# Kernel optimization log

Hardware: AMD Instinct MI355X
Metric: run time of the kernel (lower is better)

## Reference

```python
import jax, jax.numpy as jnp
import numpy as np

N_WIN = 7
NUM_HEADS = 8
DIM = 256
QK = 256
TOPK = 4
MLP_HID = 4 * DIM
SCALE = QK ** -0.5  # used for both region routing and pixel attention (qk_scale=None)


def _layernorm(x, g, b, eps=1e-6):
    mu = jnp.mean(x, axis=-1, keepdims=True)
    var = jnp.mean(jnp.square(x - mu), axis=-1, keepdims=True)
    return (x - mu) * jax.lax.rsqrt(var + eps) * g + b


def _dwconv(x, w, b):
    # x: NHWC, w: (5,5,1,C) depthwise kernel (torch Conv2d groups=C, padding=2)
    y = jax.lax.conv_general_dilated(
        x, w, window_strides=(1, 1), padding='SAME',
        feature_group_count=x.shape[-1],
        dimension_numbers=('NHWC', 'HWIO', 'NHWC'))
    return y + b


def _bra(x, qkv_w, qkv_b, lepe_w, lepe_b, wo_w, wo_b):
    # BiLevelRoutingAttention, NHWC in/out
    N, H, W, C = x.shape
    j = i = N_WIN
    h, w = H // j, W // i
    p2, w2, m = j * i, h * w, NUM_HEADS
    dq, dv = QK // m, C // m
    # window partition: (N, p2, h, w, C)
    xw = x.reshape(N, j, h, i, w, C).transpose(0, 1, 3, 2, 4, 5).reshape(N, p2, h, w, C)
    qkv = xw @ qkv_w + qkv_b
    q = qkv[..., :QK]            # (N,p2,h,w,QK)
    kv = qkv[..., QK:]           # (N,p2,h,w,QK+C)
    q_pix = q.reshape(N, p2, w2, QK)
    kv_pix = kv.reshape(N, p2, w2, QK + C)
    q_win = jnp.mean(q, axis=(2, 3))                    # (N,p2,QK)
    k_win = jnp.mean(kv[..., :QK], axis=(2, 3))         # (N,p2,QK)
    # LePE: depthwise conv on V in full-image layout
    v_img = kv[..., QK:].reshape(N, j, i, h, w, C).transpose(0, 1, 3, 2, 4, 5).reshape(N, H, W, C)
    lepe = _dwconv(v_img, lepe_w, lepe_b)
    # region-to-region routing, top-k window selection
    logit = jnp.einsum('npc,nqc->npq', q_win * SCALE, k_win)    # (N,p2,p2)
    _, r_idx = jax.lax.top_k(logit, TOPK)                       # (N,p2,TOPK)
    # gather KV of selected windows: (N,p2,TOPK,w2,QK+C)
    kv_sel = kv_pix[jnp.arange(N)[:, None, None], r_idx]
    k_sel = kv_sel[..., :QK].reshape(N, p2, TOPK * w2, m, dq).transpose(0, 1, 3, 2, 4)  # (N,p2,m,kw2,dq)
    v_sel = kv_sel[..., QK:].reshape(N, p2, TOPK * w2, m, dv).transpose(0, 1, 3, 2, 4)  # (N,p2,m,kw2,dv)
    q_h = q_pix.reshape(N, p2, w2, m, dq).transpose(0, 1, 3, 2, 4)                      # (N,p2,m,w2,dq)
    aw = jnp.einsum('npmqd,npmkd->npmqk', q_h * SCALE, k_sel)
    aw = jax.nn.softmax(aw, axis=-1)
    out = jnp.einsum('npmqk,npmkd->npmqd', aw, v_sel)           # (N,p2,m,w2,dv)
    out = out.transpose(0, 1, 3, 2, 4).reshape(N, j, i, h, w, C)
    out = out.transpose(0, 1, 3, 2, 4, 5).reshape(N, H, W, C)
    out = out + lepe
    return out @ wo_w + wo_b


def setup_inputs() -> dict:
    key = jax.random.key(0)
    ks = jax.random.split(key, 8)
    s = 0.02
    return {
        'x': jax.random.normal(ks[0], (8, 56, 56, DIM), dtype=jnp.float32),
        'ln1_g': jnp.ones((DIM,), jnp.float32),
        'ln1_b': jnp.zeros((DIM,), jnp.float32),
        'qkv_w': jax.random.normal(ks[1], (DIM, 2 * QK + DIM), jnp.float32) * s,
        'qkv_b': jnp.zeros((2 * QK + DIM,), jnp.float32),
        'lepe_w': jax.random.normal(ks[2], (5, 5, 1, DIM), jnp.float32) * s,
        'lepe_b': jnp.zeros((DIM,), jnp.float32),
        'wo_w': jax.random.normal(ks[3], (DIM, DIM), jnp.float32) * s,
        'wo_b': jnp.zeros((DIM,), jnp.float32),
        'ln2_g': jnp.ones((DIM,), jnp.float32),
        'ln2_b': jnp.zeros((DIM,), jnp.float32),
        'mlp_w1': jax.random.normal(ks[4], (DIM, MLP_HID), jnp.float32) * s,
        'mlp_b1': jnp.zeros((MLP_HID,), jnp.float32),
        'mlp_w2': jax.random.normal(ks[5], (MLP_HID, DIM), jnp.float32) * s,
        'mlp_b2': jnp.zeros((DIM,), jnp.float32),
    }


def reference(x, ln1_g, ln1_b, qkv_w, qkv_b, lepe_w, lepe_b, wo_w, wo_b,
              ln2_g, ln2_b, mlp_w1, mlp_b1, mlp_w2, mlp_b2):
    x = x + _bra(_layernorm(x, ln1_g, ln1_b), qkv_w, qkv_b, lepe_w, lepe_b, wo_w, wo_b)
    h = _layernorm(x, ln2_g, ln2_b)
    h = jax.nn.gelu(h @ mlp_w1 + mlp_b1, approximate=False) @ mlp_w2 + mlp_b2
    return x + h
```

## Files before the change

kernel.cpp:

```cpp
#include <hip/hip_runtime.h>
#include <hip/hip_bf16.h>

#define NIMG 8
#define HW 56
#define CDIM 256
#define TOK (NIMG*HW*HW)
#define NWIN 49
#define NPW (NIMG*NWIN)
#define ATT_SCALE 0.0625f

typedef __attribute__((ext_vector_type(8))) short short8;
typedef __attribute__((ext_vector_type(4))) short short4v;
typedef __attribute__((ext_vector_type(4))) float f32x4;

static const size_t OFF_WQKV  = 0;
static const size_t OFF_WWO   = 393216;
static const size_t OFF_W1    = 524288;
static const size_t OFF_W2    = 1048576;
static const size_t OFF_XLN   = 1572864;
static const size_t OFF_QKV   = 14417920;
static const size_t OFF_QKWIN = 52953088;
static const size_t OFF_RIDX  = 53755904;
static const size_t OFF_ATTN  = 53762176;

__device__ __forceinline__ float gelu_exact(float v) {
    return 0.5f * v * (1.f + erff(v * 0.70710678118654752f));
}
__device__ __forceinline__ short f2bs(float x) {
    __hip_bfloat16 h = __float2bfloat16(x);
    return *(short*)&h;
}
__device__ __forceinline__ float bs2f(short s) {
    return __uint_as_float(((unsigned)(unsigned short)s) << 16);
}
__device__ __forceinline__ void gld16(const short* g, short* l) {
    __builtin_amdgcn_global_load_lds(
        (const __attribute__((address_space(1))) void*)g,
        (__attribute__((address_space(3))) void*)l, 16, 0, 0);
}

__global__ __launch_bounds__(256) void transpose_cast4_k(const float* __restrict__ s0,
                                                         const float* __restrict__ s1,
                                                         const float* __restrict__ s2,
                                                         const float* __restrict__ s3,
                                                         __hip_bfloat16* __restrict__ d0,
                                                         __hip_bfloat16* __restrict__ d1,
                                                         __hip_bfloat16* __restrict__ d2,
                                                         __hip_bfloat16* __restrict__ d3) {
    int b = blockIdx.x;
    const float* src; __hip_bfloat16* dst; int K, N, l;
    if (b < 192)      { src = s0; dst = d0; K = 256;  N = 768;  l = b; }
    else if (b < 256) { src = s1; dst = d1; K = 256;  N = 256;  l = b - 192; }
    else if (b < 512) { src = s2; dst = d2; K = 256;  N = 1024; l = b - 256; }
    else              { src = s3; dst = d3; K = 1024; N = 256;  l = b - 512; }
    int nx = N / 32;
    int n0 = (l % nx) * 32, k0 = (l / nx) * 32;
    __shared__ float t[32][33];
    int tx = threadIdx.x & 31, ty = threadIdx.x >> 5;
    #pragma unroll
    for (int i = 0; i < 32; i += 8)
        t[ty + i][tx] = src[(size_t)(k0 + ty + i) * N + n0 + tx];
    __syncthreads();
    #pragma unroll
    for (int i = 0; i < 32; i += 8)
        dst[(size_t)(n0 + ty + i) * K + k0 + tx] = __float2bfloat16(t[tx][ty + i]);
}

__global__ __launch_bounds__(256) void ln_bf_k(const float* __restrict__ in,
                                               const float* __restrict__ g,
                                               const float* __restrict__ b,
                                               short* __restrict__ out, int remap) {
    int t = blockIdx.x * 4 + (threadIdx.x >> 6);
    int lane = threadIdx.x & 63;
    float4 v = *(const float4*)(in + (size_t)t * 256 + lane * 4);
    float s = v.x + v.y + v.z + v.w;
    float s2 = v.x * v.x + v.y * v.y + v.z * v.z + v.w * v.w;
    #pragma unroll
    for (int o = 32; o > 0; o >>= 1) {
        s  += __shfl_xor(s, o);
        s2 += __shfl_xor(s2, o);
    }
    float mu = s * (1.f / 256.f);
    float rstd = rsqrtf(s2 * (1.f / 256.f) - mu * mu + 1e-6f);
    float4 gv = *(const float4*)(g + lane * 4);
    float4 bv = *(const float4*)(b + lane * 4);
    short4v o;
    o[0] = f2bs((v.x - mu) * rstd * gv.x + bv.x);
    o[1] = f2bs((v.y - mu) * rstd * gv.y + bv.y);
    o[2] = f2bs((v.z - mu) * rstd * gv.z + bv.z);
    o[3] = f2bs((v.w - mu) * rstd * gv.w + bv.w);
    size_t tb;
    if (remap) {
        int n = t / 3136, rem = t % 3136, y = rem / 56, x = rem % 56;
        int p = (y >> 3) * 7 + (x >> 3);
        int si = (y & 7) * 8 + (x & 7);
        tb = (size_t)(n * 49 + p) * 64 + si;
    } else {
        tb = (size_t)t;
    }
    *(short4v*)(out + tb * 256 + lane * 4) = o;
}

__device__ __forceinline__ void mfma_step(const short* As, const short* Bs,
                                          int wm, int wn, int l15, int swr,
                                          f32x4 acc[2][4]) {
    short8 af[2], bfr[4];
    #pragma unroll
    for (int i = 0; i < 2; ++i)
        af[i] = *(const short8*)&As[(wm + i * 16 + l15) * 32 + swr];
    #pragma unroll
    for (int j = 0; j < 4; ++j)
        bfr[j] = *(const short8*)&Bs[(wn + j * 16 + l15) * 32 + swr];
    #pragma unroll
    for (int i = 0; i < 2; ++i)
        #pragma unroll
        for (int j = 0; j < 4; ++j)
            acc[i][j] = __builtin_amdgcn_mfma_f32_16x16x32_bf16(af[i], bfr[j], acc[i][j], 0, 0, 0);
}

template<int MODE>
__global__ __launch_bounds__(256) void gemm64(const short* __restrict__ A,
                                              const short* __restrict__ Bt,
                                              const float* __restrict__ bias,
                                              const float* __restrict__ res,
                                              void* Cv, float* __restrict__ winptr,
                                              int M, int N, int K) {
    const int bn = blockIdx.x * 128;
    const int bm = blockIdx.y * 64;
    const int tid = threadIdx.x;
    const int wave = tid >> 6, lane = tid & 63;
    const int l15 = lane & 15, quad = lane >> 4;
    const int wm = (wave & 1) * 32, wn = (wave >> 1) * 64;

    __shared__ __align__(16) short smem[18432];

    f32x4 acc[2][4];
    #pragma unroll
    for (int i = 0; i < 2; ++i)
        #pragma unroll
        for (int j = 0; j < 4; ++j) acc[i][j] = (f32x4){0.f, 0.f, 0.f, 0.f};

    const int srow = lane >> 2;
    const int scg  = ((lane & 3) ^ ((lane >> 3) & 3)) * 8;
    const short* ga  = A  + (size_t)(bm + wave * 16 + srow) * K + scg;
    const short* gb0 = Bt + (size_t)(bn + wave * 16 + srow) * K + scg;
    const short* gb1 = gb0 + (size_t)64 * K;
    const int swr = (quad ^ ((l15 >> 1) & 3)) * 8;

    const int nt = K >> 5;

    {
        short* b0 = smem;
        gld16(ga,       b0 + wave * 512);
        gld16(gb0,      b0 + 2048 + wave * 512);
        gld16(gb1,      b0 + 4096 + wave * 512);
        short* b1 = smem + 6144;
        gld16(ga  + 32, b1 + wave * 512);
        gld16(gb0 + 32, b1 + 2048 + wave * 512);
        gld16(gb1 + 32, b1 + 4096 + wave * 512);
    }

    for (int t = 0; t < nt; ++t) {
        if (t == nt - 1) asm volatile("s_waitcnt vmcnt(0)" ::: "memory");
        else             asm volatile("s_waitcnt vmcnt(3)" ::: "memory");
        __builtin_amdgcn_s_barrier();
        asm volatile("" ::: "memory");
        if (t + 2 < nt) {
            short* b = smem + ((t + 2) % 3) * 6144;
            int kk = (t + 2) * 32;
            gld16(ga  + kk, b + wave * 512);
            gld16(gb0 + kk, b + 2048 + wave * 512);
            gld16(gb1 + kk, b + 4096 + wave * 512);
        }
        const short* As = smem + (t % 3) * 6144;
        mfma_step(As, As + 2048, wm, wn, l15, swr, acc);
    }

    if (MODE == 0) {
        if (bn < 512) {
            float* wmean = (float*)&smem[12288];
            #pragma unroll
            for (int j = 0; j < 4; ++j) {
                float s = 0.f;
                #pragma unroll
                for (int i = 0; i < 2; ++i)
                    #pragma unroll
                    for (int r = 0; r < 4; ++r) s += acc[i][j][r];
                s += __shfl_xor(s, 16);
                s += __shfl_xor(s, 32);
                if (quad == 0) wmean[wave * 64 + j * 16 + l15] = s;
            }
            __syncthreads();
            if (tid < 128) {
                int c = tid;
                float s = (c < 64) ? (wmean[c] + wmean[64 + c])
                                   : (wmean[64 + c] + wmean[128 + c]);
                int col = bn + c;
                if (col < 512)
                    winptr[(size_t)blockIdx.y * 512 + col] = s * (1.f / 64.f) + bias[col];
            }
        }
    }

    if (MODE == 1) {
        #pragma unroll
        for (int i = 0; i < 2; ++i) {
            int row = bm + wm + i * 16 + quad * 4;
            #pragma unroll
            for (int j = 0; j < 4; ++j) {
                int col = bn + wn + j * 16 + l15;
                float bia = bias[col];
                #pragma unroll
                for (int r = 0; r < 4; ++r) {
                    size_t idx = (size_t)(row + r) * N + col;
                    ((float*)Cv)[idx] = acc[i][j][r] + bia + res[idx];
                }
            }
        }
    } else {
        asm volatile("s_waitcnt lgkmcnt(0)" ::: "memory");
        __builtin_amdgcn_s_barrier();
        asm volatile("" ::: "memory");
        float biasv[4];
        #pragma unroll
        for (int j = 0; j < 4; ++j) biasv[j] = bias[bn + wn + j * 16 + l15];
        short* ep = &smem[wave * 1280];
        short* outp = (short*)Cv;
        #pragma unroll
        for (int p = 0; p < 2; ++p) {
            #pragma unroll
            for (int i = 0; i < 2; ++i)
                #pragma unroll
                for (int jj = 0; jj < 2; ++jj) {
                    int j = p * 2 + jj;
                    #pragma unroll
                    for (int r = 0; r < 4; ++r) {
                        float v = acc[i][j][r] + biasv[j];
                        if (MODE == 2) v = gelu_exact(v);
                        ep[(i * 16 + quad * 4 + r) * 40 + jj * 16 + l15] = f2bs(v);
                    }
                }
            __builtin_amdgcn_s_waitcnt(0);
            int c = lane & 3;
            #pragma unroll
            for (int rr = 0; rr < 2; ++rr) {
                int row = rr * 16 + (lane >> 2);
                short8 v = *(const short8*)&ep[row * 40 + c * 8];
                *(short8*)&outp[(size_t)(bm + wm + row) * N + bn + wn + p * 32 + c * 8] = v;
            }
            __builtin_amdgcn_s_waitcnt(0);
        }
    }
}

__global__ __launch_bounds__(256) void gemm_woln_k(const short* __restrict__ A,
                                                   const short* __restrict__ Bt,
                                                   const float* __restrict__ bias,
                                                   const float* __restrict__ res,
                                                   const float* __restrict__ g2,
                                                   const float* __restrict__ b2,
                                                   float* __restrict__ out,
                                                   short* __restrict__ h2) {
    const int K = 256;
    const int bm = blockIdx.x * 64;
    const int tid = threadIdx.x;
    const int wave = tid >> 6, lane = tid & 63;
    const int l15 = lane & 15, quad = lane >> 4;
    const int wn = wave * 64;

    __shared__ __align__(16) short smem[30720];

    f32x4 acc[4][4];
    #pragma unroll
    for (int i = 0; i < 4; ++i)
        #pragma unroll
        for (int j = 0; j < 4; ++j) acc[i][j] = (f32x4){0.f, 0.f, 0.f, 0.f};

    const int srow = lane >> 2;
    const int scg  = ((lane & 3) ^ ((lane >> 3) & 3)) * 8;
    const short* ga  = A  + (size_t)(bm + wave * 16 + srow) * K + scg;
    const short* gb  = Bt + (size_t)(wn + srow) * K + scg;
    const int swr = (quad ^ ((l15 >> 1) & 3)) * 8;

    const int nt = 8;

    #define WOLN_STAGE(T) do {                                              \
        short* _b = smem + ((T) % 3) * 10240;                               \
        int _kk = (T) * 32;                                                 \
        gld16(ga + _kk, _b + wave * 512);                                   \
        _Pragma("unroll")                                                   \
        for (int X = 0; X < 4; ++X)                                         \
            gld16(gb + (size_t)X * 16 * K + _kk,                            \
                  _b + 2048 + (wave * 4 + X) * 512);                        \
    } while (0)

    WOLN_STAGE(0);
    WOLN_STAGE(1);

    for (int t = 0; t < nt; ++t) {
        if (t == nt - 1) asm volatile("s_waitcnt vmcnt(0)" ::: "memory");
        else             asm volatile("s_waitcnt vmcnt(5)" ::: "memory");
        __builtin_amdgcn_s_barrier();
        asm volatile("" ::: "memory");
        if (t + 2 < nt) WOLN_STAGE(t + 2);
        const short* As = smem + (t % 3) * 10240;
        const short* Bs = As + 2048;
        short8 af[4], bfr[4];
        #pragma unroll
        for (int i = 0; i < 4; ++i)
            af[i] = *(const short8*)&As[(i * 16 + l15) * 32 + swr];
        #pragma unroll
        for (int j = 0; j < 4; ++j)
            bfr[j] = *(const short8*)&Bs[(wn + j * 16 + l15) * 32 + swr];
        #pragma unroll
        for (int i = 0; i < 4; ++i)
            #pragma unroll
            for (int j = 0; j < 4; ++j)
                acc[i][j] = __builtin_amdgcn_mfma_f32_16x16x32_bf16(af[i], bfr[j], acc[i][j], 0, 0, 0);
    }
    #undef WOLN_STAGE

    float bv4[4];
    #pragma unroll
    for (int j = 0; j < 4; ++j) bv4[j] = bias[wn + j * 16 + l15];
    #pragma unroll
    for (int i = 0; i < 4; ++i) {
        int row = bm + i * 16 + quad * 4;
        #pragma unroll
        for (int j = 0; j < 4; ++j) {
            int col = wn + j * 16 + l15;
            #pragma unroll
            for (int r = 0; r < 4; ++r) {
                size_t idx = (size_t)(row + r) * 256 + col;
                float y = acc[i][j][r] + bv4[j] + res[idx];
                out[idx] = y;
                acc[i][j][r] = y;
            }
        }
    }

    float* S1 = (float*)smem;
    float* S2 = (float*)smem + 256;
    #pragma unroll
    for (int i = 0; i < 4; ++i) {
        #pragma unroll
        for (int r = 0; r < 4; ++r) {
            float s1 = 0.f, s2 = 0.f;
            #pragma unroll
            for (int j = 0; j < 4; ++j) {
                float y = acc[i][j][r];
                s1 += y; s2 += y * y;
            }
            #pragma unroll
            for (int o = 1; o < 16; o <<= 1) {
                s1 += __shfl_xor(s1, o);
                s2 += __shfl_xor(s2, o);
            }
            if (l15 == 0) {
                int R = i * 16 + quad * 4 + r;
                S1[wave * 64 + R] = s1;
                S2[wave * 64 + R] = s2;
            }
        }
    }
    __syncthreads();

    float gv4[4], bb4[4];
    #pragma unroll
    for (int j = 0; j < 4; ++j) {
        gv4[j] = g2[wn + j * 16 + l15];
        bb4[j] = b2[wn + j * 16 + l15];
    }
    #pragma unroll
    for (int i = 0; i < 4; ++i) {
        #pragma unroll
        for (int r = 0; r < 4; ++r) {
            int R = i * 16 + quad * 4 + r;
            float t1 = S1[R] + S1[64 + R] + S1[128 + R] + S1[192 + R];
            float t2 = S2[R] + S2[64 + R] + S2[128 + R] + S2[192 + R];
            float mu = t1 * (1.f / 256.f);
            float rstd = rsqrtf(t2 * (1.f / 256.f) - mu * mu + 1e-6f);
            #pragma unroll
            for (int j = 0; j < 4; ++j) {
                int col = wn + j * 16 + l15;
                h2[(size_t)(bm + R) * 256 + col] =
                    f2bs((acc[i][j][r] - mu) * rstd * gv4[j] + bb4[j]);
            }
        }
    }
}

__global__ __launch_bounds__(256) void mlp_fused_k(const short* __restrict__ h2,
                                                   const short* __restrict__ w1t,
                                                   const float* __restrict__ b1,
                                                   const short* __restrict__ w2t,
                                                   const float* __restrict__ b2,
                                                   float* __restrict__ out) {
    const int bm = blockIdx.x * 64;
    const int tid = threadIdx.x;
    const int wave = tid >> 6, lane = tid & 63;
    const int l15 = lane & 15, quad = lane >> 4;
    const int wm = (wave & 1) * 32, wn = (wave >> 1) * 64;
    const int wn2 = wave * 64;

    __shared__ __align__(16) short smem[32768];
    short* G   = smem;
    short* stg = smem + 16384;

    f32x4 acc2[4][4];
    #pragma unroll
    for (int i = 0; i < 4; ++i)
        #pragma unroll
        for (int j = 0; j < 4; ++j) acc2[i][j] = (f32x4){0.f, 0.f, 0.f, 0.f};

    const int srow = lane >> 2;
    const int scg  = ((lane & 3) ^ ((lane >> 3) & 3)) * 8;
    const int swr  = (quad ^ ((l15 >> 1) & 3)) * 8;
    const int sg   = (l15 & 3) ^ (l15 >> 2);
    const short* gA = h2 + (size_t)(bm + wave * 16 + srow) * 256 + scg;

    for (int Q = 0; Q < 4; ++Q) {
        for (int ch = 0; ch < 2; ++ch) {
            const int H0 = Q * 256 + ch * 128;
            const short* gB0 = w1t + (size_t)(H0 + wave * 16 + srow) * 256 + scg;
            const short* gB1 = gB0 + (size_t)64 * 256;
            gld16(gA,  stg + wave * 512);
            gld16(gB0, stg + 2048 + wave * 512);
            gld16(gB1, stg + 4096 + wave * 512);
            f32x4 acc1[2][4];
            #pragma unroll
            for (int i = 0; i < 2; ++i)
                #pragma unroll
                for (int j = 0; j < 4; ++j) acc1[i][j] = (f32x4){0.f, 0.f, 0.f, 0.f};
            for (int t = 0; t < 8; ++t) {
                __syncthreads();
                if (t + 1 < 8) {
                    short* b = stg + ((t + 1) & 1) * 6144;
                    int kk = (t + 1) * 32;
                    gld16(gA  + kk, b + wave * 512);
                    gld16(gB0 + kk, b + 2048 + wave * 512);
                    gld16(gB1 + kk, b + 4096 + wave * 512);
                }
                const short* As = stg + (t & 1) * 6144;
                mfma_step(As, As + 2048, wm, wn, l15, swr, acc1);
            }
            float b1v[4];
            #pragma unroll
            for (int j = 0; j < 4; ++j) b1v[j] = b1[H0 + wn + j * 16 + l15];
            #pragma unroll
            for (int i = 0; i < 2; ++i) {
                int row = wm + i * 16 + quad * 4;
                #pragma unroll
                for (int j = 0; j < 4; ++j) {
                    int colL = ch * 128 + wn + j * 16 + l15;
                    #pragma unroll
                    for (int r = 0; r < 4; ++r) {
                        int rw = row + r;
                        int sw = r ^ quad;
                        int cs = (colL & ~31) | ((((colL >> 3) & 3) ^ sw) << 3) | (colL & 7);
                        G[rw * 256 + cs] = f2bs(gelu_exact(acc1[i][j][r] + b1v[j]));
                    }
                }
            }
            __syncthreads();
        }

        {
            const short* gW = w2t + (size_t)(wn2 + srow) * 1024 + Q * 256 + scg;
            #pragma unroll
            for (int X = 0; X < 4; ++X)
                gld16(gW + (size_t)X * 16 * 1024, stg + (wave * 4 + X) * 512);
            for (int s = 0; s < 8; ++s) {
                __builtin_amdgcn_s_waitcnt(0);
                if (s + 1 < 8) {
                    short* b = stg + ((s + 1) & 1) * 8192;
                    int kk = (s + 1) * 32;
                    #pragma unroll
                    for (int X = 0; X < 4; ++X)
                        gld16(gW + (size_t)X * 16 * 1024 + kk, b + (wave * 4 + X) * 512);
                }
                const short* Bs = stg + (s & 1) * 8192;
                short8 af[4], bfr[4];
                #pragma unroll
                for (int i = 0; i < 4; ++i)
                    af[i] = *(const short8*)&G[(i * 16 + l15) * 256 + s * 32 + ((quad ^ sg) << 3)];
                #pragma unroll
                for (int j = 0; j < 4; ++j)
                    bfr[j] = *(const short8*)&Bs[(wave * 4 + j) * 512 + l15 * 32 + swr];
                #pragma unroll
                for (int i = 0; i < 4; ++i)
                    #pragma unroll
                    for (int j = 0; j < 4; ++j)
                        acc2[i][j] = __builtin_amdgcn_mfma_f32_16x16x32_bf16(af[i], bfr[j], acc2[i][j], 0, 0, 0);
            }
            __syncthreads();
        }
    }

    float b2v[4];
    #pragma unroll
    for (int j = 0; j < 4; ++j) b2v[j] = b2[wn2 + j * 16 + l15];
    #pragma unroll
    for (int i = 0; i < 4; ++i) {
        int row = bm + i * 16 + quad * 4;
        #pragma unroll
        for (int j = 0; j < 4; ++j) {
            int col = wn2 + j * 16 + l15;
            #pragma unroll
            for (int r = 0; r < 4; ++r) {
                size_t idx = (size_t)(row + r) * 256 + col;
                out[idx] = acc2[i][j][r] + b2v[j] + out[idx];
            }
        }
    }
}

__global__ __launch_bounds__(64) void route_k(const float* __restrict__ qkwin,
                                              int* __restrict__ ridx) {
    int w = blockIdx.x;
    int n = w / 49;
    int tid = threadIdx.x;
    __shared__ float qv[256];
    __shared__ float lg[49];
    for (int i = tid; i < 256; i += 64) qv[i] = qkwin[(size_t)w * 512 + i] * ATT_SCALE;
    __syncthreads();
    if (tid < 49) {
        const float* kp = qkwin + (size_t)(n * 49 + tid) * 512 + 256;
        float d = 0.f;
        for (int cc = 0; cc < 256; ++cc) d += qv[cc] * kp[cc];
        lg[tid] = d;
    }
    __syncthreads();
    if (tid == 0) {
        #pragma unroll
        for (int t = 0; t < 4; ++t) {
            float best = -1e30f; int bi = 0;
            for (int j = 0; j < 49; ++j)
                if (lg[j] > best) { best = lg[j]; bi = j; }
            lg[bi] = -1e30f;
            ridx[w * 4 + t] = bi;
        }
    }
}

__global__ __launch_bounds__(256) void attn_mfma_k(const short* __restrict__ qkv,
                                                   const int* __restrict__ ridx,
                                                   short* __restrict__ attn) {
    const int blk = blockIdx.x;
    const int w = blk >> 3, h = blk & 7;
    const int n = w / 49;
    const int tid = threadIdx.x;
    const int wave = tid >> 6, lane = tid & 63;
    const int l15 = lane & 15, quad = lane >> 4;

    __shared__ __align__(16) short smem[25344];
    short* Vt = smem;
    short* Ks = smem + 8448;
    short* Ps = smem + 8448;
    __shared__ int rs4[4];
    if (tid < 4) rs4[tid] = ridx[w * 4 + tid];
    __syncthreads();

    {
        int s = tid >> 2, kq = (tid & 3) * 8;
        #pragma unroll
        for (int u = 0; u < 4; ++u) {
            int key = u * 64 + s;
            const short* src = qkv + ((size_t)(n * 49 + rs4[u]) * 64 + s) * 768 + 256 + h * 32 + kq;
            *(short8*)&Ks[key * 40 + kq] = *(const short8*)src;
        }
    }
    {
        int kp = tid & 127, dh = tid >> 7;
        int k0 = kp * 2;
        int t = k0 >> 6, s = k0 & 63;
        const short* src0 = qkv + ((size_t)(n * 49 + rs4[t]) * 64 + s) * 768 + 512 + h * 32 + dh * 16;
        const short* src1 = src0 + 768;
        short8 a0 = *(const short8*)src0, a1 = *(const short8*)(src0 + 8);
        short8 b0 = *(const short8*)src1, b1 = *(const short8*)(src1 + 8);
        #pragma unroll
        for (int d = 0; d < 8; ++d) {
            *(unsigned*)&Vt[(dh * 16 + d) * 264 + k0] =
                (unsigned)(unsigned short)a0[d] | ((unsigned)(unsigned short)b0[d] << 16);
            *(unsigned*)&Vt[(dh * 16 + 8 + d) * 264 + k0] =
                (unsigned)(unsigned short)a1[d] | ((unsigned)(unsigned short)b1[d] << 16);
        }
    }
    __syncthreads();

    const short* qp = qkv + ((size_t)w * 64 + wave * 16 + l15) * 768 + h * 32 + quad * 8;
    short8 qf = *(const short8*)qp;

    f32x4 st[16];
    #pragma unroll
    for (int j = 0; j < 16; ++j) {
        short8 kf = *(const short8*)&Ks[(j * 16 + l15) * 40 + quad * 8];
        st[j] = __builtin_amdgcn_mfma_f32_16x16x32_bf16(kf, qf, (f32x4){0.f, 0.f, 0.f, 0.f}, 0, 0, 0);
    }

    float mx = -1e30f;
    #pragma unroll
    for (int j = 0; j < 16; ++j)
        #pragma unroll
        for (int r = 0; r < 4; ++r) mx = fmaxf(mx, st[j][r]);
    mx = fmaxf(mx, __shfl_xor(mx, 16));
    mx = fmaxf(mx, __shfl_xor(mx, 32));

    __syncthreads();

    short* pw = &Ps[wave * 16 * 264];
    float sum = 0.f;
    #pragma unroll
    for (int j = 0; j < 16; ++j) {
        short4v pv;
        #pragma unroll
        for (int r = 0; r < 4; ++r) {
            float p = __expf((st[j][r] - mx) * ATT_SCALE);
            sum += p;
            pv[r] = f2bs(p);
        }
        *(short4v*)&pw[l15 * 264 + j * 16 + quad * 4] = pv;
    }
    sum += __shfl_xor(sum, 16);
    sum += __shfl_xor(sum, 32);
    float inv = 1.f / sum;
    __builtin_amdgcn_s_waitcnt(0);

    f32x4 oc[2] = {(f32x4){0.f,0.f,0.f,0.f}, (f32x4){0.f,0.f,0.f,0.f}};
    #pragma unroll
    for (int kk = 0; kk < 8; ++kk) {
        short8 pf = *(const short8*)&pw[l15 * 264 + kk * 32 + quad * 8];
        #pragma unroll
        for (int jj = 0; jj < 2; ++jj) {
            short8 vf = *(const short8*)&Vt[(jj * 16 + l15) * 264 + kk * 32 + quad * 8];
            oc[jj] = __builtin_amdgcn_mfma_f32_16x16x32_bf16(vf, pf, oc[jj], 0, 0, 0);
        }
    }

    short* op = attn + ((size_t)w * 64 + wave * 16 + l15) * 256 + h * 32;
    #pragma unroll
    for (int jj = 0; jj < 2; ++jj) {
        short4v o4;
        #pragma unroll
        for (int r = 0; r < 4; ++r) o4[r] = f2bs(oc[jj][r] * inv);
        *(short4v*)&op[jj * 16 + quad * 4] = o4;
    }
}

__global__ __launch_bounds__(256) void lepe_k(const short* __restrict__ qkv,
                                              const short* __restrict__ attn,
                                              const float* __restrict__ lw,
                                              const float* __restrict__ lb,
                                              short* __restrict__ ywo) {
    int t = blockIdx.x * 8 + (threadIdx.x >> 5);
    int c0 = (threadIdx.x & 31) * 8;
    int n = t / 3136, rem = t % 3136, y = rem / 56, x = rem % 56;
    float sum[8];
    {
        float4 b0 = *(const float4*)(lb + c0), b1 = *(const float4*)(lb + c0 + 4);
        sum[0] = b0.x; sum[1] = b0.y; sum[2] = b0.z; sum[3] = b0.w;
        sum[4] = b1.x; sum[5] = b1.y; sum[6] = b1.z; sum[7] = b1.w;
    }
    #pragma unroll
    for (int ky = 0; ky < 5; ++ky) {
        int yy = y + ky - 2;
        if ((unsigned)yy >= 56u) continue;
        #pragma unroll
        for (int kx = 0; kx < 5; ++kx) {
            int xx = x + kx - 2;
            if ((unsigned)xx >= 56u) continue;
            int p = (yy >> 3) * 7 + (xx >> 3);
            int si = (yy & 7) * 8 + (xx & 7);
            short8 v = *(const short8*)(qkv + ((size_t)(n * 49 + p) * 64 + si) * 768 + 512 + c0);
            const float* wp = lw + (ky * 5 + kx) * 256 + c0;
            float4 w0 = *(const float4*)wp, w1 = *(const float4*)(wp + 4);
            sum[0] += bs2f(v[0]) * w0.x; sum[1] += bs2f(v[1]) * w0.y;
            sum[2] += bs2f(v[2]) * w0.z; sum[3] += bs2f(v[3]) * w0.w;
            sum[4] += bs2f(v[4]) * w1.x; sum[5] += bs2f(v[5]) * w1.y;
            sum[6] += bs2f(v[6]) * w1.z; sum[7] += bs2f(v[7]) * w1.w;
        }
    }
    int p0 = (y >> 3) * 7 + (x >> 3);
    int s0 = (y & 7) * 8 + (x & 7);
    short8 a = *(const short8*)(attn + ((size_t)(n * 49 + p0) * 64 + s0) * 256 + c0);
    short8 o;
    #pragma unroll
    for (int i = 0; i < 8; ++i) o[i] = f2bs(sum[i] + bs2f(a[i]));
    *(short8*)(ywo + (size_t)t * 256 + c0) = o;
}

extern "C" void kernel_launch(void* const* d_in, const int* in_sizes, int n_in,
                              void* d_out, int out_size, void* d_ws, size_t ws_size,
                              hipStream_t stream) {
    const float* x      = (const float*)d_in[0];
    const float* ln1_g  = (const float*)d_in[1];
    const float* ln1_b  = (const float*)d_in[2];
    const float* qkv_w  = (const float*)d_in[3];
    const float* qkv_b  = (const float*)d_in[4];
    const float* lepe_w = (const float*)d_in[5];
    const float* lepe_b = (const float*)d_in[6];
    const float* wo_w   = (const float*)d_in[7];
    const float* wo_b   = (const float*)d_in[8];
    const float* ln2_g  = (const float*)d_in[9];
    const float* ln2_b  = (const float*)d_in[10];
    const float* mlp_w1 = (const float*)d_in[11];
    const float* mlp_b1 = (const float*)d_in[12];
    const float* mlp_w2 = (const float*)d_in[13];
    const float* mlp_b2 = (const float*)d_in[14];
    float* out = (float*)d_out;

    char* ws = (char*)d_ws;
    __hip_bfloat16* wqkvT = (__hip_bfloat16*)(ws + OFF_WQKV);
    __hip_bfloat16* wwoT  = (__hip_bfloat16*)(ws + OFF_WWO);
    __hip_bfloat16* w1T   = (__hip_bfloat16*)(ws + OFF_W1);
    __hip_bfloat16* w2T   = (__hip_bfloat16*)(ws + OFF_W2);
    short* xln   = (short*)(ws + OFF_XLN);
    short* qkvb  = (short*)(ws + OFF_QKV);
    float* qkwin = (float*)(ws + OFF_QKWIN);
    int*   ridx  = (int*)(ws + OFF_RIDX);
    short* attnb = (short*)(ws + OFF_ATTN);
    short* ywo   = (short*)(ws + OFF_XLN);
    short* h2    = (short*)(ws + OFF_ATTN);

    transpose_cast4_k<<<768, 256, 0, stream>>>(qkv_w, wo_w, mlp_w1, mlp_w2,
                                               wqkvT, wwoT, w1T, w2T);
    ln_bf_k<<<TOK/4, 256, 0, stream>>>(x, ln1_g, ln1_b, xln, 1);
    gemm64<0><<<dim3(6, 392), 256, 0, stream>>>(xln, (const short*)wqkvT,
                                                qkv_b, nullptr, qkvb, qkwin, TOK, 768, 256);
    route_k<<<NPW, 64, 0, stream>>>(qkwin, ridx);
    attn_mfma_k<<<NPW * 8, 256, 0, stream>>>(qkvb, ridx, attnb);
    lepe_k<<<TOK/8, 256, 0, stream>>>(qkvb, attnb, lepe_w, lepe_b, ywo);
    gemm_woln_k<<<TOK/64, 256, 0, stream>>>(ywo, (const short*)wwoT, wo_b, x,
                                            ln2_g, ln2_b, out, h2);
    mlp_fused_k<<<TOK/64, 256, 0, stream>>>(h2, (const short*)w1T, mlp_b1,
                                            (const short*)w2T, mlp_b2, out);
}
```

Before: 275.8 us.

## Restructure fused MLP into two 32-row halves with LDS-resident activation tile

The fused MLP kernel now processes its 64-row block as two 32-row halves. Each half loads the h2 activation rows into swizzled LDS once and reuses them across all hidden chunks. The first GEMM now gives each wave a 256-wide hidden slice via per-wave weight staging without block barriers, in place of the old shared A/B staging with __syncthreads each k-step. This halves the accumulator register footprint and removes redundant h2 reloads and barriers, but w1/w2 weights are now streamed twice per block, doubling weight traffic.

```diff
diff --git a/kernel.cpp b/kernel.cpp
--- a/kernel.cpp
+++ b/kernel.cpp
@@ -400,118 +400,142 @@
     const int tid = threadIdx.x;
     const int wave = tid >> 6, lane = tid & 63;
     const int l15 = lane & 15, quad = lane >> 4;
-    const int wm = (wave & 1) * 32, wn = (wave >> 1) * 64;
     const int wn2 = wave * 64;
 
     __shared__ __align__(16) short smem[32768];
-    short* G   = smem;
+    short* Ah  = smem;
+    short* G   = smem + 8192;
     short* stg = smem + 16384;
-
-    f32x4 acc2[4][4];
-    #pragma unroll
-    for (int i = 0; i < 4; ++i)
-        #pragma unroll
-        for (int j = 0; j < 4; ++j) acc2[i][j] = (f32x4){0.f, 0.f, 0.f, 0.f};
 
     const int srow = lane >> 2;
     const int scg  = ((lane & 3) ^ ((lane >> 3) & 3)) * 8;
     const int swr  = (quad ^ ((l15 >> 1) & 3)) * 8;
     const int sg   = (l15 & 3) ^ (l15 >> 2);
-    const short* gA = h2 + (size_t)(bm + wave * 16 + srow) * 256 + scg;
-
-    for (int Q = 0; Q < 4; ++Q) {
-        for (int ch = 0; ch < 2; ++ch) {
-            const int H0 = Q * 256 + ch * 128;
-            const short* gB0 = w1t + (size_t)(H0 + wave * 16 + srow) * 256 + scg;
-            const short* gB1 = gB0 + (size_t)64 * 256;
-            gld16(gA,  stg + wave * 512);
-            gld16(gB0, stg + 2048 + wave * 512);
-            gld16(gB1, stg + 4096 + wave * 512);
-            f32x4 acc1[2][4];
-            #pragma unroll
-            for (int i = 0; i < 2; ++i)
-                #pragma unroll
-                for (int j = 0; j < 4; ++j) acc1[i][j] = (f32x4){0.f, 0.f, 0.f, 0.f};
-            for (int t = 0; t < 8; ++t) {
-                __syncthreads();
-                if (t + 1 < 8) {
-                    short* b = stg + ((t + 1) & 1) * 6144;
-                    int kk = (t + 1) * 32;
-                    gld16(gA  + kk, b + wave * 512);
-                    gld16(gB0 + kk, b + 2048 + wave * 512);
-                    gld16(gB1 + kk, b + 4096 + wave * 512);
+
+    float b2v[4];
+    #pragma unroll
+    for (int j = 0; j < 4; ++j) b2v[j] = b2[wn2 + j * 16 + l15];
+
+    for (int H = 0; H < 2; ++H) {
+        #pragma unroll
+        for (int v = 0; v < 4; ++v) {
+            int s8 = v * 256 + tid;
+            int row = s8 >> 5;
+            int col0 = (s8 & 31) * 8;
+            short8 val = *(const short8*)&h2[(size_t)(bm + H * 32 + row) * 256 + col0];
+            int key = (row & 3) ^ ((row >> 2) & 3);
+            int cs = (col0 & ~31) | ((((col0 >> 3) & 3) ^ key) << 3);
+            *(short8*)&Ah[row * 256 + cs] = val;
+        }
+        __syncthreads();
+
+        f32x4 acc2[2][4];
+        #pragma unroll
+        for (int i = 0; i < 2; ++i)
+            #pragma unroll
+            for (int j = 0; j < 4; ++j) acc2[i][j] = (f32x4){0.f, 0.f, 0.f, 0.f};
+
+        for (int Q = 0; Q < 4; ++Q) {
+            {
+                const short* gW = w1t + (size_t)(Q * 256 + wn2 + srow) * 256 + scg;
+                #pragma unroll
+                for (int X = 0; X < 4; ++X)
+                    gld16(gW + (size_t)X * 16 * 256, stg + (wave * 4 + X) * 512);
+                f32x4 acc1[2][4];
+                #pragma unroll
+                for (int i = 0; i < 2; ++i)
+                    #pragma unroll
+                    for (int j = 0; j < 4; ++j) acc1[i][j] = (f32x4){0.f, 0.f, 0.f, 0.f};
+                for (int t = 0; t < 8; ++t) {
+                    __builtin_amdgcn_s_waitcnt(0);
+                    if (t + 1 < 8) {
+                        short* b = stg + ((t + 1) & 1) * 8192;
+                        int kk = (t + 1) * 32;
+                        #pragma unroll
+                        for (int X = 0; X < 4; ++X)
+                            gld16(gW + (size_t)X * 16 * 256 + kk, b + (wave * 4 + X) * 512);
+                    }
+                    const short* Bs = stg + (t & 1) * 8192;
+                    short8 af[2], bfr[4];
+                    #pragma unroll
+                    for (int i = 0; i < 2; ++i)
+                        af[i] = *(const short8*)&Ah[(i * 16 + l15) * 256 + t * 32 + ((quad ^ sg) << 3)];
+                    #pragma unroll
+                    for (int j = 0; j < 4; ++j)
+                        bfr[j] = *(const short8*)&Bs[(wave * 4 + j) * 512 + l15 * 32 + swr];
+                    #pragma unroll
+                    for (int i = 0; i < 2; ++i)
+                        #pragma unroll
+                        for (int j = 0; j < 4; ++j)
+                            acc1[i][j] = __builtin_amdgcn_mfma_f32_16x16x32_bf16(af[i], bfr[j], acc1[i][j], 0, 0, 0);
                 }
-                const short* As = stg + (t & 1) * 6144;
-                mfma_step(As, As + 2048, wm, wn, l15, swr, acc1);
-            }
-            float b1v[4];
-            #pragma unroll
-            for (int j = 0; j < 4; ++j) b1v[j] = b1[H0 + wn + j * 16 + l15];
-            #pragma unroll
-            for (int i = 0; i < 2; ++i) {
-                int row = wm + i * 16 + quad * 4;
-                #pragma unroll
-                for (int j = 0; j < 4; ++j) {
-                    int colL = ch * 128 + wn + j * 16 + l15;
-                    #pragma unroll
-                    for (int r = 0; r < 4; ++r) {
-                        int rw = row + r;
-                        int sw = r ^ quad;
-                        int cs = (colL & ~31) | ((((colL >> 3) & 3) ^ sw) << 3) | (colL & 7);
-                        G[rw * 256 + cs] = f2bs(gelu_exact(acc1[i][j][r] + b1v[j]));
+                float b1v[4];
+                #pragma unroll
+                for (int j = 0; j < 4; ++j) b1v[j] = b1[Q * 256 + wn2 + j * 16 + l15];
+                #pragma unroll
+                for (int i = 0; i < 2; ++i) {
+                    int rowb = i * 16 + quad * 4;
+                    #pragma unroll
+                    for (int j = 0; j < 4; ++j) {
+                        int colL = wn2 + j * 16 + l15;
+                        #pragma unroll
+                        for (int r = 0; r < 4; ++r) {
+                            int rw = rowb + r;
+                            int sw = r ^ quad;
+                            int cs = (colL & ~31) | ((((colL >> 3) & 3) ^ sw) << 3) | (colL & 7);
+                            G[rw * 256 + cs] = f2bs(gelu_exact(acc1[i][j][r] + b1v[j]));
+                        }
                     }
                 }
             }
             __syncthreads();
-        }
-
-        {
-            const short* gW = w2t + (size_t)(wn2 + srow) * 1024 + Q * 256 + scg;
-            #pragma unroll
-            for (int X = 0; X < 4; ++X)
-                gld16(gW + (size_t)X * 16 * 1024, stg + (wave * 4 + X) * 512);
-            for (int s = 0; s < 8; ++s) {
-                __builtin_amdgcn_s_waitcnt(0);
-                if (s + 1 < 8) {
-                    short* b = stg + ((s + 1) & 1) * 8192;
-                    int kk = (s + 1) * 32;
-                    #pragma unroll
-                    for (int X = 0; X < 4; ++X)
-                        gld16(gW + (size_t)X * 16 * 1024 + kk, b + (wave * 4 + X) * 512);
+
+            {
+                const short* gW = w2t + (size_t)(wn2 + srow) * 1024 + Q * 256 + scg;
+                #pragma unroll
+                for (int X = 0; X < 4; ++X)
+                    gld16(gW + (size_t)X * 16 * 1024, stg + (wave * 4 + X) * 512);
+                for (int s = 0; s < 8; ++s) {
+                    __builtin_amdgcn_s_waitcnt(0);
+                    if (s + 1 < 8) {
+                        short* b = stg + ((s + 1) & 1) * 8192;
+                        int kk = (s + 1) * 32;
+                        #pragma unroll
+                        for (int X = 0; X < 4; ++X)
+                            gld16(gW + (size_t)X * 16 * 1024 + kk, b + (wave * 4 + X) * 512);
+                    }
+                    const short* Bs = stg + (s & 1) * 8192;
+                    short8 af[2], bfr[4];
+                    #pragma unroll
+                    for (int i = 0; i < 2; ++i)
+                        af[i] = *(const short8*)&G[(i * 16 + l15) * 256 + s * 32 + ((quad ^ sg) << 3)];
+                    #pragma unroll
+                    for (int j = 0; j < 4; ++j)
+                        bfr[j] = *(const short8*)&Bs[(wave * 4 + j) * 512 + l15 * 32 + swr];
+                    #pragma unroll
+                    for (int i = 0; i < 2; ++i)
+                        #pragma unroll
+                        for (int j = 0; j < 4; ++j)
+                            acc2[i][j] = __builtin_amdgcn_mfma_f32_16x16x32_bf16(af[i], bfr[j], acc2[i][j], 0, 0, 0);
                 }
-                const short* Bs = stg + (s & 1) * 8192;
-                short8 af[4], bfr[4];
-                #pragma unroll
-                for (int i = 0; i < 4; ++i)
-                    af[i] = *(const short8*)&G[(i * 16 + l15) * 256 + s * 32 + ((quad ^ sg) << 3)];
-                #pragma unroll
-                for (int j = 0; j < 4; ++j)
-                    bfr[j] = *(const short8*)&Bs[(wave * 4 + j) * 512 + l15 * 32 + swr];
-                #pragma unroll
-                for (int i = 0; i < 4; ++i)
-                    #pragma unroll
-                    for (int j = 0; j < 4; ++j)
-                        acc2[i][j] = __builtin_amdgcn_mfma_f32_16x16x32_bf16(af[i], bfr[j], acc2[i][j], 0, 0, 0);
             }
             __syncthreads();
         }
-    }
-
-    float b2v[4];
-    #pragma unroll
-    for (int j = 0; j < 4; ++j) b2v[j] = b2[wn2 + j * 16 + l15];
-    #pragma unroll
-    for (int i = 0; i < 4; ++i) {
-        int row = bm + i * 16 + quad * 4;
-        #pragma unroll
-        for (int j = 0; j < 4; ++j) {
-            int col = wn2 + j * 16 + l15;
-            #pragma unroll
-            for (int r = 0; r < 4; ++r) {
-                size_t idx = (size_t)(row + r) * 256 + col;
-                out[idx] = acc2[i][j][r] + b2v[j] + out[idx];
-            }
-        }
+
+        #pragma unroll
+        for (int i = 0; i < 2; ++i) {
+            int row = bm + H * 32 + i * 16 + quad * 4;
+            #pragma unroll
+            for (int j = 0; j < 4; ++j) {
+                int col = wn2 + j * 16 + l15;
+                #pragma unroll
+                for (int r = 0; r < 4; ++r) {
+                    size_t idx = (size_t)(row + r) * 256 + col;
+                    out[idx] = acc2[i][j][r] + b2v[j] + out[idx];
+                }
+            }
+        }
+        __syncthreads();
     }
 }
 
```

New measurement: 286.9 us. 1.04x slower.
